# Optimization experiments

Measured on AMD Instinct MI355X. Metric: run time of the kernel, lower is better.

The kernel has to match this reference:

```python
import jax, jax.numpy as jnp
import numpy as np
import math

H, W, R = 100, 100, 2          # BEV grid and neighbor range
K = (2 * R + 1) ** 2           # 25 spatial neighbors
C = 256                        # input_dim == hidden_dim
NH, DK = 8, 32                 # heads, head dim
T = 5                          # temporal history length
NEG = -1e10                    # mask fill value from the source


def build_neighbors():
    # Clamped (2R+1)x(2R+1) window per pixel (faithful to the intent of
    # generate_spatial_neighbors: edge pixels reuse the nearest interior window).
    hs = np.clip(np.arange(H), R, H - 1 - R)
    ws = np.clip(np.arange(W), R, W - 1 - R)
    off = np.arange(-R, R + 1)
    rows = hs[:, None] + off[None, :]                      # [H, 2R+1]
    cols = ws[:, None] + off[None, :]                      # [W, 2R+1]
    idx = rows[:, None, :, None] * W + cols[None, :, None, :]  # [H,W,2R+1,2R+1]
    return idx.reshape(H * W, K).astype(np.int32)


def setup_inputs() -> dict:
    key = jax.random.key(0)
    ks = jax.random.split(key, 40)
    N = H * W
    inp = {"x": jax.random.normal(ks[0], (N, T, C), jnp.float32)}
    i = 1
    for pfx in ("t", "s"):
        for nm in ("q", "k", "v", "o"):
            inp[f"{pfx}_W{nm}"] = jax.random.normal(ks[i], (C, C), jnp.float32) * 0.02; i += 1
            inp[f"{pfx}_b{nm}"] = jax.random.normal(ks[i], (C,), jnp.float32) * 0.02; i += 1
    inp["neighbors"] = jnp.asarray(build_neighbors())
    inp["tmask"] = jnp.ones((N, 1, T), jnp.int32)
    inp["smask"] = jnp.ones((N, 1, K), jnp.int32)
    return inp


def _heads(x, Wx, b):
    # x: [N, L, C] -> [N, NH, L, DK]
    N, L, _ = x.shape
    return (x @ Wx + b).reshape(N, L, NH, DK).transpose(0, 2, 1, 3)


def _attend(q, k, v, mask4):
    # q: [N,NH,Lq,DK], k/v: [N,NH,Lk,DK], mask4: [N,1,1,Lk]
    scores = jnp.einsum('nhqd,nhkd->nhqk', q, k) / math.sqrt(q.shape[-1])
    scores = jnp.where(mask4 == 0, NEG, scores)
    p = jax.nn.softmax(scores, axis=-1)
    return jnp.einsum('nhqk,nhkd->nhqd', p, v)


def _forward(x, t_Wq, t_bq, t_Wk, t_bk, t_Wv, t_bv, t_Wo, t_bo,
             s_Wq, s_bq, s_Wk, s_bk, s_Wv, s_bv, s_Wo, s_bo,
             neighbors, tmask, smask):
    N = x.shape[0]
    # ---- temporal aggregation (MultiHeadedAttention): latest frame attends history
    q_last = x[:, -1:, :]                                   # [N,1,C]
    q = _heads(q_last, t_Wq, t_bq)                          # [N,NH,1,DK]
    k = _heads(x, t_Wk, t_bk)                               # [N,NH,T,DK]
    v = _heads(x, t_Wv, t_bv)
    ctx = _attend(q, k, v, tmask[:, None, :, :])            # [N,NH,1,DK]
    h_t = ctx.transpose(0, 2, 1, 3).reshape(N, 1, C) @ t_Wo + t_bo  # [N,1,C]
    # ---- spatial neighbor attention (MultiHeadedAttention_spatial):
    # K/V are projected from the query features, then gathered by neighbor index.
    sq = _heads(h_t, s_Wq, s_bq)                            # [N,NH,1,DK]
    k1 = h_t[:, 0, :] @ s_Wk + s_bk                          # [N,C] per-pixel key token
    v1 = h_t[:, 0, :] @ s_Wv + s_bv                          # [N,C]
    kn = k1[neighbors].reshape(N, K, NH, DK).transpose(0, 2, 1, 3)  # [N,NH,K,DK]
    vn = v1[neighbors].reshape(N, K, NH, DK).transpose(0, 2, 1, 3)
    sctx = _attend(sq, kn, vn, smask[:, None, :, :])        # [N,NH,1,DK]
    out = sctx.transpose(0, 2, 1, 3).reshape(N, 1, C) @ s_Wo + s_bo  # [N,1,C]
    return out


def reference(x, t_Wq, t_bq, t_Wk, t_bk, t_Wv, t_bv, t_Wo, t_bo,
              s_Wq, s_bq, s_Wk, s_bk, s_Wv, s_bv, s_Wo, s_bo,
              neighbors, tmask, smask):
    return _forward(x, t_Wq, t_bq, t_Wk, t_bk, t_Wv, t_bv, t_Wo, t_bo,
                    s_Wq, s_bq, s_Wk, s_bk, s_Wv, s_bv, s_Wo, s_bo,
                    neighbors, tmask, smask)
```

## Files before the change

### kernel.cpp

```cpp
#include <hip/hip_runtime.h>

constexpr int TT = 5;
constexpr int KK = 25;
#define NEGV -1e10f

typedef _Float16 f16;
typedef __attribute__((ext_vector_type(8))) _Float16 f16x8;
typedef __attribute__((ext_vector_type(4))) _Float16 f16x4;
typedef __attribute__((ext_vector_type(4))) float f32x4;

__device__ __forceinline__ void gload16(const void* g, void* l) {
    __builtin_amdgcn_global_load_lds(
        (const __attribute__((address_space(1))) unsigned int*)g,
        (__attribute__((address_space(3))) unsigned int*)l, 16, 0, 0);
}

__device__ __forceinline__ int xcd_remap(int id, int G) {
    const int c = id & 7, j = id >> 3;
    const int q = G >> 3, r = G & 7;
    const int base = (c < r) ? c * (q + 1) : r * (q + 1) + (c - r) * q;
    return base + j;
}

struct PrepArgs { const float* W[8]; const float* b[8]; };

__global__ __launch_bounds__(256) void prep_w8(
    PrepArgs pa, f16* __restrict__ wth, f16* __restrict__ wtl,
    float* __restrict__ bc)
{
    __shared__ float sT[64][65];
    const int z = blockIdx.z;
    const float* W = pa.W[z];
    f16* wh = wth + (size_t)z * 65536;
    f16* wl = wtl + (size_t)z * 65536;
    const int t  = threadIdx.x;
    const int k0 = blockIdx.x * 64, n0 = blockIdx.y * 64;
    const int kk = t >> 2;
    #pragma unroll
    for (int c = 0; c < 4; ++c) {
        const int col = (t & 3) * 16 + c * 4;
        float4 v = *(const float4*)(W + (size_t)(k0 + kk) * 256 + n0 + col);
        sT[kk][col] = v.x; sT[kk][col + 1] = v.y; sT[kk][col + 2] = v.z; sT[kk][col + 3] = v.w;
    }
    __syncthreads();
    const int n = t >> 2, ks = (t & 3) * 16;
    f16* ph = wh + (size_t)(n0 + n) * 256 + k0 + ks;
    f16* pl = wl + (size_t)(n0 + n) * 256 + k0 + ks;
    f16x8 vh, vl;
    #pragma unroll
    for (int j0 = 0; j0 < 16; j0 += 8) {
        #pragma unroll
        for (int j = 0; j < 8; ++j) {
            const float f = sT[ks + j0 + j][n];
            const f16 h = (f16)f;
            vh[j] = h;
            vl[j] = (f16)(f - (float)h);
        }
        *(f16x8*)(ph + j0) = vh;
        *(f16x8*)(pl + j0) = vl;
    }
    if (blockIdx.x == 0 && blockIdx.y == 0) bc[z * 256 + t] = pa.b[z][t];
}

__global__ __launch_bounds__(256) void cvt_x(
    const float* __restrict__ x, f16* __restrict__ xh, int n8)
{
    for (int i = blockIdx.x * 256 + threadIdx.x; i < n8; i += gridDim.x * 256) {
        const float4 a = ((const float4*)x)[2 * i];
        const float4 b = ((const float4*)x)[2 * i + 1];
        f16x8 o;
        o[0] = (f16)a.x; o[1] = (f16)a.y; o[2] = (f16)a.z; o[3] = (f16)a.w;
        o[4] = (f16)b.x; o[5] = (f16)b.y; o[6] = (f16)b.z; o[7] = (f16)b.w;
        *(f16x8*)(xh + (size_t)i * 8) = o;
    }
}

template<int OM>
__global__ __launch_bounds__(512, 4) void gemm_f16(
    const f16* __restrict__ A, int lda, int M,
    const f16* __restrict__ Wh, const f16* __restrict__ Wl,
    const float* __restrict__ bias,
    float* __restrict__ Cf, f16* __restrict__ Ch, int ldc,
    int GY, int G)
{
    __shared__ f16 sA[128 * 32], sBh[128 * 32], sBl[128 * 32];

    const int tid = threadIdx.x;
    const int l   = tid & 63, w = tid >> 6;
    const int l15 = l & 15, l4 = l >> 4;
    const int wm  = w >> 2, wn = w & 3;

    const int p  = xcd_remap(blockIdx.x, G);
    const int bm = (p / GY) * 128;
    const int bn = (p % GY) * 128;

    const int srow = l >> 2, sc = (l & 3) * 8;
    int ar = bm + w * 16 + srow;
    if (ar > M - 1) ar = M - 1;
    const size_t aoff = (size_t)ar * lda + sc;
    const size_t boff = (size_t)(bn + w * 16 + srow) * 256 + sc;
    const int sbase = w * 512;

    f32x4 acc[4][2];
    #pragma unroll
    for (int i = 0; i < 4; ++i)
        #pragma unroll
        for (int j = 0; j < 2; ++j) acc[i][j] = f32x4{0.f, 0.f, 0.f, 0.f};

    for (int k0 = 0; k0 < 256; k0 += 32) {
        gload16(A + aoff + k0, sA + sbase);
        gload16(Wh + boff + k0, sBh + sbase);
        gload16(Wl + boff + k0, sBl + sbase);
        __syncthreads();

        f16x8 a[4], bh[2], bl[2];
        #pragma unroll
        for (int mf = 0; mf < 4; ++mf)
            a[mf] = *(const f16x8*)(sA + (wm * 64 + mf * 16 + l15) * 32 + l4 * 8);
        #pragma unroll
        for (int nf = 0; nf < 2; ++nf) {
            const int r = wn * 32 + nf * 16 + l15;
            bh[nf] = *(const f16x8*)(sBh + r * 32 + l4 * 8);
            bl[nf] = *(const f16x8*)(sBl + r * 32 + l4 * 8);
        }
        #pragma unroll
        for (int mf = 0; mf < 4; ++mf)
            #pragma unroll
            for (int nf = 0; nf < 2; ++nf) {
                acc[mf][nf] = __builtin_amdgcn_mfma_f32_16x16x32_f16(a[mf], bh[nf], acc[mf][nf], 0, 0, 0);
                acc[mf][nf] = __builtin_amdgcn_mfma_f32_16x16x32_f16(a[mf], bl[nf], acc[mf][nf], 0, 0, 0);
            }
        __syncthreads();
    }

    #pragma unroll
    for (int mf = 0; mf < 4; ++mf) {
        const int row0 = bm + wm * 64 + mf * 16 + l4 * 4;
        #pragma unroll
        for (int nf = 0; nf < 2; ++nf) {
            const int col = bn + wn * 32 + nf * 16 + l15;
            const float bs = bias[col];
            #pragma unroll
            for (int i = 0; i < 4; ++i) {
                const int row = row0 + i;
                if (row < M) {
                    const float v = acc[mf][nf][i] + bs;
                    const size_t o = (size_t)row * ldc + col;
                    if (OM == 0) Cf[o] = v;
                    else         Ch[o] = (f16)v;
                }
            }
        }
    }
}

__global__ __launch_bounds__(256) void attn_t(
    const f16* __restrict__ q, const f16* __restrict__ kv,
    const int* __restrict__ tmask, f16* __restrict__ ctx)
{
    const int tid = threadIdx.x;
    const int wv = tid >> 6, l = tid & 63;
    const int n = blockIdx.x * 4 + wv;
    const int col = ((l >> 3) * 32) + (l & 7) * 4;
    const float scale = 0.1767766952966369f;

    const f16x4 qv = *(const f16x4*)(q + (size_t)n * 256 + col);
    const float q0 = (float)qv[0], q1 = (float)qv[1], q2 = (float)qv[2], q3 = (float)qv[3];

    float m = -3.0e38f, lsum = 0.f;
    float a0 = 0.f, a1 = 0.f, a2 = 0.f, a3 = 0.f;
    #pragma unroll
    for (int t = 0; t < TT; ++t) {
        const size_t row = ((size_t)n * TT + t) * 512;
        const f16x4 kk = *(const f16x4*)(kv + row + col);
        const f16x4 vv = *(const f16x4*)(kv + row + 256 + col);
        float p = q0 * (float)kk[0] + q1 * (float)kk[1]
                + q2 * (float)kk[2] + q3 * (float)kk[3];
        p += __shfl_xor(p, 1);
        p += __shfl_xor(p, 2);
        p += __shfl_xor(p, 4);
        const float s  = (tmask[n * TT + t] == 0) ? NEGV : p * scale;
        const float mn = fmaxf(m, s);
        const float sc = exp2f((m - mn) * 1.44269504f);
        const float pe = exp2f((s - mn) * 1.44269504f);
        lsum = lsum * sc + pe;
        a0 = a0 * sc + pe * (float)vv[0];
        a1 = a1 * sc + pe * (float)vv[1];
        a2 = a2 * sc + pe * (float)vv[2];
        a3 = a3 * sc + pe * (float)vv[3];
        m = mn;
    }
    const float inv = 1.0f / lsum;
    f16x4 o;
    o[0] = (f16)(a0 * inv); o[1] = (f16)(a1 * inv);
    o[2] = (f16)(a2 * inv); o[3] = (f16)(a3 * inv);
    *(f16x4*)(ctx + (size_t)n * 256 + col) = o;
}

__global__ __launch_bounds__(256) void attn_s(
    const f16* __restrict__ sqkv, const int* __restrict__ nbrs,
    const int* __restrict__ smask, f16* __restrict__ sctx, int G)
{
    __shared__ int nbL[4 * KK];
    __shared__ int mkL[4 * KK];
    const int tid = threadIdx.x;
    const int nbase = xcd_remap(blockIdx.x, G) * 4;
    if (tid < 4 * KK) {
        nbL[tid] = nbrs[nbase * KK + tid];
        mkL[tid] = smask[nbase * KK + tid];
    }
    __syncthreads();

    const int wv = tid >> 6, l = tid & 63;
    const int n = nbase + wv;
    const int col = ((l >> 3) * 32) + (l & 7) * 4;
    const float scale = 0.1767766952966369f;

    const f16x4 qv = *(const f16x4*)(sqkv + (size_t)n * 768 + col);
    const float q0 = (float)qv[0], q1 = (float)qv[1], q2 = (float)qv[2], q3 = (float)qv[3];

    float m = -3.0e38f, lsum = 0.f;
    float a0 = 0.f, a1 = 0.f, a2 = 0.f, a3 = 0.f;
    #pragma unroll
    for (int j = 0; j < KK; ++j) {
        const size_t row = (size_t)nbL[wv * KK + j] * 768;
        const f16x4 kk = *(const f16x4*)(sqkv + row + 256 + col);
        const f16x4 vv = *(const f16x4*)(sqkv + row + 512 + col);
        float p = q0 * (float)kk[0] + q1 * (float)kk[1]
                + q2 * (float)kk[2] + q3 * (float)kk[3];
        p += __shfl_xor(p, 1);
        p += __shfl_xor(p, 2);
        p += __shfl_xor(p, 4);
        const float s  = (mkL[wv * KK + j] == 0) ? NEGV : p * scale;
        const float mn = fmaxf(m, s);
        const float sc = exp2f((m - mn) * 1.44269504f);
        const float pe = exp2f((s - mn) * 1.44269504f);
        lsum = lsum * sc + pe;
        a0 = a0 * sc + pe * (float)vv[0];
        a1 = a1 * sc + pe * (float)vv[1];
        a2 = a2 * sc + pe * (float)vv[2];
        a3 = a3 * sc + pe * (float)vv[3];
        m = mn;
    }
    const float inv = 1.0f / lsum;
    f16x4 o;
    o[0] = (f16)(a0 * inv); o[1] = (f16)(a1 * inv);
    o[2] = (f16)(a2 * inv); o[3] = (f16)(a3 * inv);
    *(f16x4*)(sctx + (size_t)n * 256 + col) = o;
}

extern "C" void kernel_launch(void* const* d_in, const int* in_sizes, int n_in,
                              void* d_out, int out_size, void* d_ws, size_t ws_size,
                              hipStream_t stream)
{
    const float* x = (const float*)d_in[0];
    const int* nbrs  = (const int*)d_in[17];
    const int* tmask = (const int*)d_in[18];
    const int* smask = (const int*)d_in[19];
    float* out = (float*)d_out;

    const int N  = in_sizes[0] / (TT * 256);
    const int MT = N * TT;

    f16* wth = (f16*)d_ws;
    f16* wtl = wth + (size_t)2048 * 256;
    float* bc = (float*)(wtl + (size_t)2048 * 256);
    f16* xh     = (f16*)(bc + 2048);
    f16* kvbuf  = xh + (size_t)MT * 256;
    f16* q16    = kvbuf + (size_t)MT * 512;
    f16* ctx    = q16 + (size_t)N * 256;
    f16* ht     = ctx + (size_t)N * 256;
    f16* sqkv16 = ht + (size_t)N * 256;
    f16* sctx   = sqkv16 + (size_t)N * 768;

    PrepArgs pa;
    pa.W[0] = (const float*)d_in[3];  pa.b[0] = (const float*)d_in[4];
    pa.W[1] = (const float*)d_in[5];  pa.b[1] = (const float*)d_in[6];
    pa.W[2] = (const float*)d_in[1];  pa.b[2] = (const float*)d_in[2];
    pa.W[3] = (const float*)d_in[7];  pa.b[3] = (const float*)d_in[8];
    pa.W[4] = (const float*)d_in[9];  pa.b[4] = (const float*)d_in[10];
    pa.W[5] = (const float*)d_in[11]; pa.b[5] = (const float*)d_in[12];
    pa.W[6] = (const float*)d_in[13]; pa.b[6] = (const float*)d_in[14];
    pa.W[7] = (const float*)d_in[15]; pa.b[7] = (const float*)d_in[16];
    prep_w8<<<dim3(4, 4, 8), 256, 0, stream>>>(pa, wth, wtl, bc);

    cvt_x<<<2048, 256, 0, stream>>>(x, xh, MT * 256 / 8);

    dim3 blk(512);
    const int GBM_T = (MT + 127) / 128;
    const int GBM_N = (N + 127) / 128;

    gemm_f16<1><<<GBM_T * 4, blk, 0, stream>>>(
        xh, 256, MT, wth, wtl, bc, nullptr, kvbuf, 512, 4, GBM_T * 4);
    gemm_f16<1><<<GBM_N * 2, blk, 0, stream>>>(
        xh + (TT - 1) * 256, TT * 256, N,
        wth + (size_t)512 * 256, wtl + (size_t)512 * 256, bc + 512,
        nullptr, q16, 256, 2, GBM_N * 2);
    attn_t<<<N / 4, dim3(256), 0, stream>>>(q16, kvbuf, tmask, ctx);
    gemm_f16<1><<<GBM_N * 2, blk, 0, stream>>>(
        ctx, 256, N,
        wth + (size_t)768 * 256, wtl + (size_t)768 * 256, bc + 768,
        nullptr, ht, 256, 2, GBM_N * 2);
    gemm_f16<1><<<GBM_N * 6, blk, 0, stream>>>(
        ht, 256, N,
        wth + (size_t)1024 * 256, wtl + (size_t)1024 * 256, bc + 1024,
        nullptr, sqkv16, 768, 6, GBM_N * 6);
    attn_s<<<N / 4, dim3(256), 0, stream>>>(sqkv16, nbrs, smask, sctx, N / 4);
    gemm_f16<0><<<GBM_N * 2, blk, 0, stream>>>(
        sctx, 256, N,
        wth + (size_t)1792 * 256, wtl + (size_t)1792 * 256, bc + 1792,
        out, nullptr, 256, 2, GBM_N * 2);
}
```

Measured before the change: 251.0 us.

## Drop split-f16 weight residual, double-buffer swizzled GEMM tiles, add BM=64 variant

Removes the hi/lo split of weights so every GEMM performs one MFMA per tile instead of two and loads half the weight bytes. The GEMM now stages 64-wide K chunks into double-buffered LDS with an XOR swizzle, so the next chunk loads while the current one is computed and LDS bank conflicts drop. It also adds a BM template that uses 64-row tiles for the N-row GEMMs, giving more blocks. Dropping the low-order weight correction reduces precision to plain f16 weights, which may matter for tolerance.

```diff
diff --git a/kernel.cpp b/kernel.cpp
--- a/kernel.cpp
+++ b/kernel.cpp
@@ -25,14 +25,12 @@
 struct PrepArgs { const float* W[8]; const float* b[8]; };
 
 __global__ __launch_bounds__(256) void prep_w8(
-    PrepArgs pa, f16* __restrict__ wth, f16* __restrict__ wtl,
-    float* __restrict__ bc)
+    PrepArgs pa, f16* __restrict__ wt, float* __restrict__ bc)
 {
     __shared__ float sT[64][65];
     const int z = blockIdx.z;
     const float* W = pa.W[z];
-    f16* wh = wth + (size_t)z * 65536;
-    f16* wl = wtl + (size_t)z * 65536;
+    f16* wh = wt + (size_t)z * 65536;
     const int t  = threadIdx.x;
     const int k0 = blockIdx.x * 64, n0 = blockIdx.y * 64;
     const int kk = t >> 2;
@@ -45,19 +43,12 @@
     __syncthreads();
     const int n = t >> 2, ks = (t & 3) * 16;
     f16* ph = wh + (size_t)(n0 + n) * 256 + k0 + ks;
-    f16* pl = wl + (size_t)(n0 + n) * 256 + k0 + ks;
-    f16x8 vh, vl;
     #pragma unroll
     for (int j0 = 0; j0 < 16; j0 += 8) {
-        #pragma unroll
-        for (int j = 0; j < 8; ++j) {
-            const float f = sT[ks + j0 + j][n];
-            const f16 h = (f16)f;
-            vh[j] = h;
-            vl[j] = (f16)(f - (float)h);
-        }
+        f16x8 vh;
+        #pragma unroll
+        for (int j = 0; j < 8; ++j) vh[j] = (f16)sT[ks + j0 + j][n];
         *(f16x8*)(ph + j0) = vh;
-        *(f16x8*)(pl + j0) = vl;
     }
     if (blockIdx.x == 0 && blockIdx.y == 0) bc[z * 256 + t] = pa.b[z][t];
 }
@@ -75,15 +66,17 @@
     }
 }
 
-template<int OM>
+template<int BM, int OM>
 __global__ __launch_bounds__(512, 4) void gemm_f16(
     const f16* __restrict__ A, int lda, int M,
-    const f16* __restrict__ Wh, const f16* __restrict__ Wl,
-    const float* __restrict__ bias,
+    const f16* __restrict__ W, const float* __restrict__ bias,
     float* __restrict__ Cf, f16* __restrict__ Ch, int ldc,
     int GY, int G)
 {
-    __shared__ f16 sA[128 * 32], sBh[128 * 32], sBl[128 * 32];
+    constexpr int MF   = BM / 32;
+    constexpr int ASEG = BM / 64;
+    __shared__ f16 sA[2][BM * 64];
+    __shared__ f16 sB[2][128 * 64];
 
     const int tid = threadIdx.x;
     const int l   = tid & 63, w = tid >> 6;
@@ -91,51 +84,75 @@
     const int wm  = w >> 2, wn = w & 3;
 
     const int p  = xcd_remap(blockIdx.x, G);
-    const int bm = (p / GY) * 128;
+    const int bm = (p / GY) * BM;
     const int bn = (p % GY) * 128;
 
-    const int srow = l >> 2, sc = (l & 3) * 8;
-    int ar = bm + w * 16 + srow;
-    if (ar > M - 1) ar = M - 1;
-    const size_t aoff = (size_t)ar * lda + sc;
-    const size_t boff = (size_t)(bn + w * 16 + srow) * 256 + sc;
-    const int sbase = w * 512;
-
-    f32x4 acc[4][2];
-    #pragma unroll
-    for (int i = 0; i < 4; ++i)
+    const int srow8 = l >> 3;
+    const int scol  = ((l & 7) ^ srow8) * 8;
+    size_t aoff[ASEG];
+    #pragma unroll
+    for (int j = 0; j < ASEG; ++j) {
+        int r = bm + (w * ASEG + j) * 8 + srow8;
+        if (r > M - 1) r = M - 1;
+        aoff[j] = (size_t)r * lda + scol;
+    }
+    size_t boff[2];
+    #pragma unroll
+    for (int j = 0; j < 2; ++j)
+        boff[j] = (size_t)(bn + (w * 2 + j) * 8 + srow8) * 256 + scol;
+
+    f32x4 acc[MF][2];
+    #pragma unroll
+    for (int i = 0; i < MF; ++i)
         #pragma unroll
         for (int j = 0; j < 2; ++j) acc[i][j] = f32x4{0.f, 0.f, 0.f, 0.f};
 
-    for (int k0 = 0; k0 < 256; k0 += 32) {
-        gload16(A + aoff + k0, sA + sbase);
-        gload16(Wh + boff + k0, sBh + sbase);
-        gload16(Wl + boff + k0, sBl + sbase);
-        __syncthreads();
-
-        f16x8 a[4], bh[2], bl[2];
-        #pragma unroll
-        for (int mf = 0; mf < 4; ++mf)
-            a[mf] = *(const f16x8*)(sA + (wm * 64 + mf * 16 + l15) * 32 + l4 * 8);
+    auto STAGE = [&](int buf, int k0) {
+        #pragma unroll
+        for (int j = 0; j < ASEG; ++j)
+            gload16(A + aoff[j] + k0, &sA[buf][(w * ASEG + j) * 512]);
+        #pragma unroll
+        for (int j = 0; j < 2; ++j)
+            gload16(W + boff[j] + k0, &sB[buf][(w * 2 + j) * 512]);
+    };
+
+    STAGE(0, 0);
+    __syncthreads();
+
+    const int swz = l15 & 7;
+    #pragma unroll
+    for (int t = 0; t < 4; ++t) {
+        if (t < 3) STAGE((t + 1) & 1, (t + 1) * 64);
+
+        f16x8 af[MF][2], bf[2][2];
+        #pragma unroll
+        for (int mf = 0; mf < MF; ++mf) {
+            const int r = wm * (BM / 2) + mf * 16 + l15;
+            #pragma unroll
+            for (int ks = 0; ks < 2; ++ks)
+                af[mf][ks] = *(const f16x8*)&sA[t & 1][r * 64 + (((ks * 4 + l4) ^ swz) * 8)];
+        }
         #pragma unroll
         for (int nf = 0; nf < 2; ++nf) {
             const int r = wn * 32 + nf * 16 + l15;
-            bh[nf] = *(const f16x8*)(sBh + r * 32 + l4 * 8);
-            bl[nf] = *(const f16x8*)(sBl + r * 32 + l4 * 8);
+            #pragma unroll
+            for (int ks = 0; ks < 2; ++ks)
+                bf[nf][ks] = *(const f16x8*)&sB[t & 1][r * 64 + (((ks * 4 + l4) ^ swz) * 8)];
         }
         #pragma unroll
-        for (int mf = 0; mf < 4; ++mf)
+        for (int mf = 0; mf < MF; ++mf)
             #pragma unroll
-            for (int nf = 0; nf < 2; ++nf) {
-                acc[mf][nf] = __builtin_amdgcn_mfma_f32_16x16x32_f16(a[mf], bh[nf], acc[mf][nf], 0, 0, 0);
-                acc[mf][nf] = __builtin_amdgcn_mfma_f32_16x16x32_f16(a[mf], bl[nf], acc[mf][nf], 0, 0, 0);
-            }
+            for (int nf = 0; nf < 2; ++nf)
+                #pragma unroll
+                for (int ks = 0; ks < 2; ++ks)
+                    acc[mf][nf] = __builtin_amdgcn_mfma_f32_16x16x32_f16(
+                        af[mf][ks], bf[nf][ks], acc[mf][nf], 0, 0, 0);
         __syncthreads();
     }
 
     #pragma unroll
-    for (int mf = 0; mf < 4; ++mf) {
-        const int row0 = bm + wm * 64 + mf * 16 + l4 * 4;
+    for (int mf = 0; mf < MF; ++mf) {
+        const int row0 = bm + wm * (BM / 2) + mf * 16 + l4 * 4;
         #pragma unroll
         for (int nf = 0; nf < 2; ++nf) {
             const int col = bn + wn * 32 + nf * 16 + l15;
@@ -262,9 +279,8 @@
     const int N  = in_sizes[0] / (TT * 256);
     const int MT = N * TT;
 
-    f16* wth = (f16*)d_ws;
-    f16* wtl = wth + (size_t)2048 * 256;
-    float* bc = (float*)(wtl + (size_t)2048 * 256);
+    f16* wt  = (f16*)d_ws;
+    float* bc = (float*)(wt + (size_t)2048 * 256);
     f16* xh     = (f16*)(bc + 2048);
     f16* kvbuf  = xh + (size_t)MT * 256;
     f16* q16    = kvbuf + (size_t)MT * 512;
@@ -282,32 +298,28 @@
     pa.W[5] = (const float*)d_in[11]; pa.b[5] = (const float*)d_in[12];
     pa.W[6] = (const float*)d_in[13]; pa.b[6] = (const float*)d_in[14];
     pa.W[7] = (const float*)d_in[15]; pa.b[7] = (const float*)d_in[16];
-    prep_w8<<<dim3(4, 4, 8), 256, 0, stream>>>(pa, wth, wtl, bc);
+    prep_w8<<<dim3(4, 4, 8), 256, 0, stream>>>(pa, wt, bc);
 
     cvt_x<<<2048, 256, 0, stream>>>(x, xh, MT * 256 / 8);
 
     dim3 blk(512);
     const int GBM_T = (MT + 127) / 128;
-    const int GBM_N = (N + 127) / 128;
-
-    gemm_f16<1><<<GBM_T * 4, blk, 0, stream>>>(
-        xh, 256, MT, wth, wtl, bc, nullptr, kvbuf, 512, 4, GBM_T * 4);
-    gemm_f16<1><<<GBM_N * 2, blk, 0, stream>>>(
+    const int GBM_S = (N + 63) / 64;
+
+    gemm_f16<128, 1><<<GBM_T * 4, blk, 0, stream>>>(
+        xh, 256, MT, wt, bc, nullptr, kvbuf, 512, 4, GBM_T * 4);
+    gemm_f16<64, 1><<<GBM_S * 2, blk, 0, stream>>>(
         xh + (TT - 1) * 256, TT * 256, N,
-        wth + (size_t)512 * 256, wtl + (size_t)512 * 256, bc + 512,
-        nullptr, q16, 256, 2, GBM_N * 2);
+        wt + (size_t)512 * 256, bc + 512, nullptr, q16, 256, 2, GBM_S * 2);
     attn_t<<<N / 4, dim3(256), 0, stream>>>(q16, kvbuf, tmask, ctx);
-    gemm_f16<1><<<GBM_N * 2, blk, 0, stream>>>(
-        ctx, 256, N,
-        wth + (size_t)768 * 256, wtl + (size_t)768 * 256, bc + 768,
-        nullptr, ht, 256, 2, GBM_N * 2);
-    gemm_f16<1><<<GBM_N * 6, blk, 0, stream>>>(
-        ht, 256, N,
-        wth + (size_t)1024 * 256, wtl + (size_t)1024 * 256, bc + 1024,
-        nullptr, sqkv16, 768, 6, GBM_N * 6);
+    gemm_f16<64, 1><<<GBM_S * 2, blk, 0, stream>>>(
+        ctx, 256, N, wt + (size_t)768 * 256, bc + 768,
+        nullptr, ht, 256, 2, GBM_S * 2);
+    gemm_f16<64, 1><<<GBM_S * 6, blk, 0, stream>>>(
+        ht, 256, N, wt + (size_t)1024 * 256, bc + 1024,
+        nullptr, sqkv16, 768, 6, GBM_S * 6);
     attn_s<<<N / 4, dim3(256), 0, stream>>>(sqkv16, nbrs, smask, sctx, N / 4);
-    gemm_f16<0><<<GBM_N * 2, blk, 0, stream>>>(
-        sctx, 256, N,
-        wth + (size_t)1792 * 256, wtl + (size_t)1792 * 256, bc + 1792,
-        out, nullptr, 256, 2, GBM_N * 2);
-}
+    gemm_f16<64, 0><<<GBM_S * 2, blk, 0, stream>>>(
+        sctx, 256, N, wt + (size_t)1792 * 256, bc + 1792,
+        out, nullptr, 256, 2, GBM_S * 2);
+}
```

New measurement: 227.1 us. -9.5%, faster.
